# Optimization experiments

Hardware: AMD Instinct MI355X
Metric: run time of the kernel (lower is better)

## Reference

```python
import jax, jax.numpy as jnp
import numpy as np

ANCHORS = np.array([[10.0, 13.0], [16.0, 30.0], [33.0, 23.0]], dtype=np.float32)
IMG_SIZE = 416
NUM_CLASSES = 80
NUM_ANCHORS = 3


def setup_inputs() -> dict:
    key = jax.random.key(0)
    B, G = 64, 52
    C = NUM_ANCHORS * (NUM_CLASSES + 5)  # 255
    x = jax.random.normal(key, (B, C, G, G), dtype=jnp.float32)
    return {"x": x}


def reference(x) -> jnp.ndarray:
    B = x.shape[0]
    G = x.shape[2]
    stride = IMG_SIZE / G
    # [B, A, 5+C, G, G] -> [B, A, G, G, 5+C]
    pred = x.reshape(B, NUM_ANCHORS, NUM_CLASSES + 5, G, G).transpose(0, 1, 3, 4, 2)
    tx = jax.nn.sigmoid(pred[..., 0])
    ty = jax.nn.sigmoid(pred[..., 1])
    tw = pred[..., 2]
    th = pred[..., 3]
    conf = jax.nn.sigmoid(pred[..., 4])
    cls = jax.nn.sigmoid(pred[..., 5:])
    # grid offsets: np.meshgrid(g, g) -> a varies along last axis (cx), b along rows (cy)
    g = jnp.arange(G, dtype=jnp.float32)
    cx = g[None, None, None, :]  # [1,1,1,G]
    cy = g[None, None, :, None]  # [1,1,G,1]
    scaled = jnp.asarray(ANCHORS) / stride  # [A,2]
    aw = scaled[:, 0][None, :, None, None]
    ah = scaled[:, 1][None, :, None, None]
    bbox = jnp.stack(
        [tx + cx, ty + cy, jnp.exp(tw) * aw, jnp.exp(th) * ah], axis=-1
    )  # [B,A,G,G,4]
    bbox_ = bbox.reshape(B, -1, 4) * stride
    conf_ = conf.reshape(B, -1, 1)
    cls_ = cls.reshape(B, -1, NUM_CLASSES)
    return jnp.concatenate([bbox_, conf_, cls_], axis=-1)  # [B, A*G*G, 5+C]
```

## Files before the change

kernel.cpp:

```cpp
#include <hip/hip_runtime.h>


#define GG   2704
#define CH   85
#define TS   52
#define LSTR 53

__global__ __launch_bounds__(256) void det_kernel(const float* __restrict__ in,
                                                  float* __restrict__ out) {
    __shared__ float lds[CH * LSTR];

    const int tile = blockIdx.x;
    const int a    = blockIdx.y;
    const int b    = blockIdx.z;
    const int tid  = threadIdx.x;

    const float4* in4 = (const float4*)(in + ((size_t)b * 255 + (size_t)a * 85) * GG
                                           + (size_t)tile * TS);
    for (int l = tid; l < CH * (TS / 4); l += 256) {
        int c  = l / 13;
        int s4 = l - c * 13;
        float4 v = in4[c * 676 + s4];
        float* dst = &lds[c * LSTR + s4 * 4];
        dst[0] = v.x; dst[1] = v.y; dst[2] = v.z; dst[3] = v.w;
    }
    __syncthreads();

    if (tid < 255) {
        const int e  = tid % 85;
        const int s0 = tid / 85;

        const float AW[3] = {10.f, 16.f, 33.f};
        const float AH[3] = {13.f, 30.f, 23.f};

        const bool  isexp = (e == 2) | (e == 3);
        const float sgn   = isexp ? 1.f : -1.f;
        float scale;
        if (e < 2)       scale = 8.f;
        else if (e == 2) scale = AW[a];
        else if (e == 3) scale = AH[a];
        else             scale = 1.f;
        float addend = (e == 0) ? 8.f * (float)s0
                     : (e == 1) ? 8.f * (float)tile : 0.f;
        const float adelta = (e == 0) ? 24.f : 0.f;

        float* op = out + ((size_t)((b * 3 + a) * GG) + (size_t)tile * TS) * CH;
        int idx = e * LSTR + s0;

        #pragma unroll 2
        for (int o = tid; o < TS * CH; o += 255, idx += 3) {
            float v = lds[idx];
            float t = __expf(sgn * v);
            float w = isexp ? t : __builtin_amdgcn_rcpf(1.f + t);
            op[o] = fmaf(scale, w, addend);
            addend += adelta;
        }
    }
}

extern "C" void kernel_launch(void* const* d_in, const int* in_sizes, int n_in,
                              void* d_out, int out_size, void* d_ws, size_t ws_size,
                              hipStream_t stream) {
    const float* x = (const float*)d_in[0];
    float* out = (float*)d_out;
    dim3 grid(52, 3, 64);
    det_kernel<<<grid, 256, 0, stream>>>(x, out);
}
```

Before: 304.5 us.

## Process four grid rows per block with 512 threads

```diff
diff --git a/kernel.cpp b/kernel.cpp
--- a/kernel.cpp
+++ b/kernel.cpp
@@ -3,11 +3,13 @@
 
 #define GG   2704
 #define CH   85
-#define TS   52
-#define LSTR 53
+#define R    4
+#define SP   (R * 52)
+#define LSTR 209
+#define NT   512
 
-__global__ __launch_bounds__(256) void det_kernel(const float* __restrict__ in,
-                                                  float* __restrict__ out) {
+__global__ __launch_bounds__(NT) void det_kernel(const float* __restrict__ in,
+                                                 float* __restrict__ out) {
     __shared__ float lds[CH * LSTR];
 
     const int tile = blockIdx.x;
@@ -16,19 +18,31 @@
     const int tid  = threadIdx.x;
 
     const float4* in4 = (const float4*)(in + ((size_t)b * 255 + (size_t)a * 85) * GG
-                                           + (size_t)tile * TS);
-    for (int l = tid; l < CH * (TS / 4); l += 256) {
-        int c  = l / 13;
-        int s4 = l - c * 13;
-        float4 v = in4[c * 676 + s4];
-        float* dst = &lds[c * LSTR + s4 * 4];
-        dst[0] = v.x; dst[1] = v.y; dst[2] = v.z; dst[3] = v.w;
+                                           + (size_t)tile * SP);
+    {
+        int l = tid;
+        #pragma unroll
+        for (int k = 0; k < 8; ++k) {
+            const int c  = l / 52;
+            const int s4 = l - c * 52;
+            const float4 v = in4[c * 676 + s4];
+            float* dst = &lds[c * LSTR + (s4 << 2)];
+            dst[0] = v.x; dst[1] = v.y; dst[2] = v.z; dst[3] = v.w;
+            l += NT;
+        }
+        if (l < CH * (SP / 4)) {
+            const int c  = l / 52;
+            const int s4 = l - c * 52;
+            const float4 v = in4[c * 676 + s4];
+            float* dst = &lds[c * LSTR + (s4 << 2)];
+            dst[0] = v.x; dst[1] = v.y; dst[2] = v.z; dst[3] = v.w;
+        }
     }
     __syncthreads();
 
-    if (tid < 255) {
-        const int e  = tid % 85;
-        const int s0 = tid / 85;
+    if (tid < 510) {
+        const int e = tid % 85;
+        int s       = tid / 85;
 
         const float AW[3] = {10.f, 16.f, 33.f};
         const float AH[3] = {13.f, 30.f, 23.f};
@@ -40,20 +54,24 @@
         else if (e == 2) scale = AW[a];
         else if (e == 3) scale = AH[a];
         else             scale = 1.f;
-        float addend = (e == 0) ? 8.f * (float)s0
-                     : (e == 1) ? 8.f * (float)tile : 0.f;
-        const float adelta = (e == 0) ? 24.f : 0.f;
+        const float cx8   = (e == 0) ? 8.f : 0.f;
+        const float cy8   = (e == 1) ? 8.f : 0.f;
+        const float ybase = (float)(tile * R);
 
-        float* op = out + ((size_t)((b * 3 + a) * GG) + (size_t)tile * TS) * CH;
-        int idx = e * LSTR + s0;
+        float* op = out + ((size_t)((b * 3 + a) * GG) + (size_t)tile * SP) * CH;
 
+        int x  = s;
+        int yl = 0;
         #pragma unroll 2
-        for (int o = tid; o < TS * CH; o += 255, idx += 3) {
-            float v = lds[idx];
+        for (int o = tid; o < SP * CH; o += 510) {
+            float v = lds[e * LSTR + s];
             float t = __expf(sgn * v);
             float w = isexp ? t : __builtin_amdgcn_rcpf(1.f + t);
+            float addend = fmaf(cx8, (float)x, cy8 * (ybase + (float)yl));
             op[o] = fmaf(scale, w, addend);
-            addend += adelta;
+            s += 6;
+            x += 6;
+            if (x >= 52) { x -= 52; yl += 1; }
         }
     }
 }
@@ -63,6 +81,6 @@
                               hipStream_t stream) {
     const float* x = (const float*)d_in[0];
     float* out = (float*)d_out;
-    dim3 grid(52, 3, 64);
-    det_kernel<<<grid, 256, 0, stream>>>(x, out);
+    dim3 grid(13, 3, 64);
+    det_kernel<<<grid, NT, 0, stream>>>(x, out);
 }
```

New measurement: 301.4 us. About the same (-1.0%).

## Process four rows per block with register-prefetched global loads

Applied to the files above, without the earlier changes.

```diff
diff --git a/kernel.cpp b/kernel.cpp
--- a/kernel.cpp
+++ b/kernel.cpp
@@ -3,57 +3,87 @@
 
 #define GG   2704
 #define CH   85
-#define TS   52
 #define LSTR 53
+#define NT   256
+#define TPB  4
 
-__global__ __launch_bounds__(256) void det_kernel(const float* __restrict__ in,
-                                                  float* __restrict__ out) {
+__global__ __launch_bounds__(NT) void det_kernel(const float* __restrict__ in,
+                                                 float* __restrict__ out) {
     __shared__ float lds[CH * LSTR];
 
-    const int tile = blockIdx.x;
-    const int a    = blockIdx.y;
-    const int b    = blockIdx.z;
-    const int tid  = threadIdx.x;
+    const int j   = blockIdx.x;
+    const int a   = blockIdx.y;
+    const int b   = blockIdx.z;
+    const int tid = threadIdx.x;
 
     const float4* in4 = (const float4*)(in + ((size_t)b * 255 + (size_t)a * 85) * GG
-                                           + (size_t)tile * TS);
-    for (int l = tid; l < CH * (TS / 4); l += 256) {
-        int c  = l / 13;
-        int s4 = l - c * 13;
-        float4 v = in4[c * 676 + s4];
-        float* dst = &lds[c * LSTR + s4 * 4];
-        dst[0] = v.x; dst[1] = v.y; dst[2] = v.z; dst[3] = v.w;
+                                           + (size_t)j * (TPB * 52));
+
+    int g0,g1,g2,g3,g4, l0,l1,l2,l3,l4;
+    {
+        int l, c, s4;
+        l = tid;        c = l/13; s4 = l - c*13; g0 = c*676 + s4; l0 = c*LSTR + (s4<<2);
+        l = tid +   NT; c = l/13; s4 = l - c*13; g1 = c*676 + s4; l1 = c*LSTR + (s4<<2);
+        l = tid + 2*NT; c = l/13; s4 = l - c*13; g2 = c*676 + s4; l2 = c*LSTR + (s4<<2);
+        l = tid + 3*NT; c = l/13; s4 = l - c*13; g3 = c*676 + s4; l3 = c*LSTR + (s4<<2);
+        l = tid + 4*NT; c = l/13; s4 = l - c*13; g4 = c*676 + s4; l4 = c*LSTR + (s4<<2);
     }
-    __syncthreads();
+    const bool x5 = (tid < 81);
 
-    if (tid < 255) {
-        const int e  = tid % 85;
-        const int s0 = tid / 85;
+    const int e  = tid % 85;
+    const int s0 = tid / 85;
+    const float AW[3] = {10.f, 16.f, 33.f};
+    const float AH[3] = {13.f, 30.f, 23.f};
+    const bool  isexp = (e == 2) | (e == 3);
+    const float sgn   = isexp ? 1.f : -1.f;
+    float scale;
+    if (e < 2)       scale = 8.f;
+    else if (e == 2) scale = AW[a];
+    else if (e == 3) scale = AH[a];
+    else             scale = 1.f;
+    const float base0  = (e == 0) ? 8.f * (float)s0 : 0.f;
+    const float adelta = (e == 0) ? 24.f : 0.f;
+    const bool  doT    = (tid < 255);
 
-        const float AW[3] = {10.f, 16.f, 33.f};
-        const float AH[3] = {13.f, 30.f, 23.f};
+    float4 v0_, v1_, v2_, v3_, v4_;
+    v0_ = in4[g0]; v1_ = in4[g1]; v2_ = in4[g2]; v3_ = in4[g3];
+    if (x5) v4_ = in4[g4];
 
-        const bool  isexp = (e == 2) | (e == 3);
-        const float sgn   = isexp ? 1.f : -1.f;
-        float scale;
-        if (e < 2)       scale = 8.f;
-        else if (e == 2) scale = AW[a];
-        else if (e == 3) scale = AH[a];
-        else             scale = 1.f;
-        float addend = (e == 0) ? 8.f * (float)s0
-                     : (e == 1) ? 8.f * (float)tile : 0.f;
-        const float adelta = (e == 0) ? 24.f : 0.f;
+    #pragma unroll
+    for (int t = 0; t < TPB; ++t) {
+        __builtin_amdgcn_s_barrier();
 
-        float* op = out + ((size_t)((b * 3 + a) * GG) + (size_t)tile * TS) * CH;
-        int idx = e * LSTR + s0;
+        {
+            float* d;
+            d = &lds[l0]; d[0]=v0_.x; d[1]=v0_.y; d[2]=v0_.z; d[3]=v0_.w;
+            d = &lds[l1]; d[0]=v1_.x; d[1]=v1_.y; d[2]=v1_.z; d[3]=v1_.w;
+            d = &lds[l2]; d[0]=v2_.x; d[1]=v2_.y; d[2]=v2_.z; d[3]=v2_.w;
+            d = &lds[l3]; d[0]=v3_.x; d[1]=v3_.y; d[2]=v3_.z; d[3]=v3_.w;
+            if (x5) { d = &lds[l4]; d[0]=v4_.x; d[1]=v4_.y; d[2]=v4_.z; d[3]=v4_.w; }
+        }
 
-        #pragma unroll 2
-        for (int o = tid; o < TS * CH; o += 255, idx += 3) {
-            float v = lds[idx];
-            float t = __expf(sgn * v);
-            float w = isexp ? t : __builtin_amdgcn_rcpf(1.f + t);
-            op[o] = fmaf(scale, w, addend);
-            addend += adelta;
+        if (t < TPB - 1) {
+            v0_ = in4[g0 + (t+1)*13]; v1_ = in4[g1 + (t+1)*13];
+            v2_ = in4[g2 + (t+1)*13]; v3_ = in4[g3 + (t+1)*13];
+            if (x5) v4_ = in4[g4 + (t+1)*13];
+        }
+
+        asm volatile("s_waitcnt lgkmcnt(0)" ::: "memory");
+        __builtin_amdgcn_s_barrier();
+
+        if (doT) {
+            const int y = j * TPB + t;
+            float addend = base0 + ((e == 1) ? 8.f * (float)y : 0.f);
+            float* op = out + ((size_t)((b * 3 + a) * GG) + (size_t)y * 52) * CH;
+            int idx = e * LSTR + s0;
+            #pragma unroll 2
+            for (int o = tid; o < 52 * CH; o += 255, idx += 3) {
+                float v  = lds[idx];
+                float tt = __expf(sgn * v);
+                float w  = isexp ? tt : __builtin_amdgcn_rcpf(1.f + tt);
+                op[o] = fmaf(scale, w, addend);
+                addend += adelta;
+            }
         }
     }
 }
@@ -63,6 +93,6 @@
                               hipStream_t stream) {
     const float* x = (const float*)d_in[0];
     float* out = (float*)d_out;
-    dim3 grid(52, 3, 64);
-    det_kernel<<<grid, 256, 0, stream>>>(x, out);
+    dim3 grid(13, 3, 64);
+    det_kernel<<<grid, NT, 0, stream>>>(x, out);
 }
```

Result: slower. 312.7 us (+2.7%).
